# Optimization experiments

Hardware: AMD Instinct MI355X
Metric: run time of the kernel (lower is better)

## Reference

```python
import jax, jax.numpy as jnp
import numpy as np

DK = 64
DROPOUT_P = 0.1


def setup_inputs() -> dict:
    key = jax.random.key(0)
    kq, kk, kv, km = jax.random.split(key, 4)
    B, S, D = 16, 2048, 64
    q = jax.random.normal(kq, (B, S, D), dtype=jnp.float32)
    k = jax.random.normal(kk, (B, S, D), dtype=jnp.float32)
    v = jax.random.normal(kv, (B, S, D), dtype=jnp.float32)
    attn_mask = jax.random.randint(km, (S, S), 0, 2, dtype=jnp.int32)
    return {"q": q, "k": k, "v": v, "attn_mask": attn_mask}


def reference(q, k, v, attn_mask):
    # q = q / sqrt(dk)
    qs = q * (1.0 / np.sqrt(DK)).astype(np.float32)
    # dots: [B, S_q, S_k]
    dots = jnp.einsum("bqd,bkd->bqk", qs, k)
    # mask: 0 -> -inf, 1 -> 0 (additive)
    add_mask = jnp.where(attn_mask == 0, -jnp.inf, 0.0).astype(dots.dtype)
    dots = dots + add_mask  # broadcast [S,S] over batch
    attn = jax.nn.softmax(dots, axis=-1)
    # inverted dropout, train mode, fixed key for determinism
    keep = jax.random.bernoulli(jax.random.key(42), 1.0 - DROPOUT_P, attn.shape)
    attn = jnp.where(keep, attn * (1.0 / (1.0 - DROPOUT_P)), 0.0)
    out = jnp.einsum("bqk,bkd->bqd", attn, v)
    return out
```

## Files before the change

### kernel.cpp

```cpp
#include <hip/hip_runtime.h>

#define BATCH 16
#define SEQ   2048
#define DIM   64
#define TQ    64
#define TK    64
#define NTHREADS 256

typedef short bf16x8 __attribute__((ext_vector_type(8)));
typedef float f32x4 __attribute__((ext_vector_type(4)));

__device__ __forceinline__ int ldsoff(int row) {
  return row * 72 + 16 * (row >> 2);
}
#define LDS_SZ (64 * 72 + 16 * 16)

__device__ __forceinline__ unsigned tf_bits(unsigned f) {
  unsigned x0 = 0u;
  unsigned x1 = f;
  const unsigned ks1 = 42u;
  const unsigned ks2 = 0x1BD11BDAu ^ 42u;
  x1 += ks1;
#define TF_R(r) { x0 += x1; x1 = __builtin_amdgcn_alignbit(x1, x1, 32u - (r)); x1 ^= x0; }
  TF_R(13) TF_R(15) TF_R(26) TF_R(6)
  x0 += ks1; x1 += ks2 + 1u;
  TF_R(17) TF_R(29) TF_R(16) TF_R(24)
  x0 += ks2; x1 += 2u;
  TF_R(13) TF_R(15) TF_R(26) TF_R(6)
  x1 += ks1 + 3u;
  TF_R(17) TF_R(29) TF_R(16) TF_R(24)
  x0 += ks1; x1 += ks2 + 4u;
  TF_R(13) TF_R(15) TF_R(26) TF_R(6)
  x0 += ks2; x1 += 5u;
#undef TF_R
  return x0 ^ x1;
}
#define KEEP_THRESH 0xE6666600u

__device__ __forceinline__ unsigned short to_bf16(float x) {
  return (unsigned short)((__float_as_uint(x) + 0x8000u) >> 16);
}
__device__ __forceinline__ unsigned pack_bf16x2(float lo, float hi) {
  const unsigned l = (__float_as_uint(lo) + 0x8000u) >> 16;
  const unsigned h = (__float_as_uint(hi) + 0x8000u) & 0xFFFF0000u;
  return h | l;
}

__global__ __launch_bounds__(NTHREADS, 2)
void attn_fwd(const float* __restrict__ q, const float* __restrict__ k,
              const float* __restrict__ v, const int* __restrict__ mask,
              float* __restrict__ out) {
  __shared__ unsigned short KS[LDS_SZ];
  __shared__ unsigned short VT[LDS_SZ];
  __shared__ unsigned short PS[LDS_SZ];

  const int t    = threadIdx.x;
  const int w    = t >> 6;
  const int lane = t & 63;
  const int tx   = lane & 15;
  const int quad = lane >> 4;
  const int bb   = blockIdx.x >> 5;
  const int q0   = (blockIdx.x & 31) * TQ;
  const int qw   = q0 + 16 * w;

  const float qscale = 0.125f * 1.44269504088896340736f;

  bf16x8 aq[2];
  {
    const float* qr = q + ((size_t)bb * SEQ + qw + tx) * DIM + quad * 8;
#pragma unroll
    for (int ks = 0; ks < 2; ++ks) {
      const float4 f0 = *(const float4*)(qr + ks * 32);
      const float4 f1 = *(const float4*)(qr + ks * 32 + 4);
      union { unsigned u[4]; bf16x8 v; } a;
      a.u[0] = pack_bf16x2(f0.x * qscale, f0.y * qscale);
      a.u[1] = pack_bf16x2(f0.z * qscale, f0.w * qscale);
      a.u[2] = pack_bf16x2(f1.x * qscale, f1.y * qscale);
      a.u[3] = pack_bf16x2(f1.z * qscale, f1.w * qscale);
      aq[ks] = a.v;
    }
  }

  float mrun[4] = {-3.0e4f, -3.0e4f, -3.0e4f, -3.0e4f};
  float lrun[4] = {0.f, 0.f, 0.f, 0.f};
  f32x4 oacc[4];
#pragma unroll
  for (int nt = 0; nt < 4; ++nt) oacc[nt] = (f32x4){0.f, 0.f, 0.f, 0.f};

  const int srow0 = t >> 4;
  const int sdd   = (t & 15) * 4;
  const float* kb = k + (size_t)bb * SEQ * DIM;
  const float* vb = v + (size_t)bb * SEQ * DIM;

  float4 kreg[4], vreg[4];
#pragma unroll
  for (int p = 0; p < 4; ++p) {
    const int rr = p * 16 + srow0;
    kreg[p] = *(const float4*)(kb + (size_t)rr * DIM + sdd);
    vreg[p] = *(const float4*)(vb + (size_t)rr * DIM + sdd);
  }

  const int* mbase = mask + (size_t)(qw + quad * 4) * SEQ + tx;
  const unsigned fbase0 = (unsigned)(bb * SEQ + qw + quad * 4) * (unsigned)SEQ + (unsigned)tx;

#pragma unroll 1
  for (int kt = 0; kt < SEQ / TK; ++kt) {
    const int k0 = kt * TK;

    __syncthreads();

#pragma unroll
    for (int p = 0; p < 4; ++p) {
      const int rr = p * 16 + srow0;
      ushort4 kk4;
      kk4.x = to_bf16(kreg[p].x); kk4.y = to_bf16(kreg[p].y);
      kk4.z = to_bf16(kreg[p].z); kk4.w = to_bf16(kreg[p].w);
      *(ushort4*)&KS[ldsoff(rr) + sdd] = kk4;
      VT[ldsoff(sdd + 0) + rr] = to_bf16(vreg[p].x);
      VT[ldsoff(sdd + 1) + rr] = to_bf16(vreg[p].y);
      VT[ldsoff(sdd + 2) + rr] = to_bf16(vreg[p].z);
      VT[ldsoff(sdd + 3) + rr] = to_bf16(vreg[p].w);
    }
    __syncthreads();

    if (kt + 1 < SEQ / TK) {
      const size_t off = (size_t)(k0 + TK) * DIM;
#pragma unroll
      for (int p = 0; p < 4; ++p) {
        const int rr = p * 16 + srow0;
        kreg[p] = *(const float4*)(kb + off + (size_t)rr * DIM + sdd);
        vreg[p] = *(const float4*)(vb + off + (size_t)rr * DIM + sdd);
      }
    }

    int mv[4][4];
    const int* mp0 = mbase + k0;
#pragma unroll
    for (int reg = 0; reg < 4; ++reg)
#pragma unroll
      for (int nt = 0; nt < 4; ++nt)
        mv[nt][reg] = mp0[(size_t)reg * SEQ + nt * 16];

    f32x4 qk[4];
#pragma unroll
    for (int nt = 0; nt < 4; ++nt) {
      f32x4 c = (f32x4){0.f, 0.f, 0.f, 0.f};
#pragma unroll
      for (int ks = 0; ks < 2; ++ks) {
        const bf16x8 b = *(const bf16x8*)&KS[ldsoff(nt * 16 + tx) + ks * 32 + quad * 8];
        c = __builtin_amdgcn_mfma_f32_16x16x32_bf16(aq[ks], b, c, 0, 0, 0);
      }
      qk[nt] = c;
    }

    float al[4];
#pragma unroll
    for (int reg = 0; reg < 4; ++reg) {
#pragma unroll
      for (int nt = 0; nt < 4; ++nt)
        qk[nt][reg] = mv[nt][reg] ? qk[nt][reg] : -1e30f;
      float mx = fmaxf(fmaxf(qk[0][reg], qk[1][reg]), fmaxf(qk[2][reg], qk[3][reg]));
      mx = fmaxf(mx, __shfl_xor(mx, 1));
      mx = fmaxf(mx, __shfl_xor(mx, 2));
      mx = fmaxf(mx, __shfl_xor(mx, 4));
      mx = fmaxf(mx, __shfl_xor(mx, 8));
      const float mn = fmaxf(mrun[reg], mx);
      al[reg] = __builtin_amdgcn_exp2f(mrun[reg] - mn);
      mrun[reg] = mn;
    }

    const unsigned fb = fbase0 + (unsigned)k0;
#pragma unroll
    for (int reg = 0; reg < 4; ++reg) {
      const float mn = mrun[reg];
      const int prow = ldsoff(16 * w + quad * 4 + reg);
      float ls = 0.0f;
#pragma unroll
      for (int nt = 0; nt < 4; ++nt) {
        const float e = __builtin_amdgcn_exp2f(qk[nt][reg] - mn);
        ls += e;
        const unsigned bits = tf_bits(fb + (unsigned)(reg * SEQ + nt * 16));
        const float pd = (bits < KEEP_THRESH) ? e : 0.0f;
        PS[prow + nt * 16 + tx] = to_bf16(pd);
      }
      lrun[reg] = lrun[reg] * al[reg] + ls;
    }

#pragma unroll
    for (int nt = 0; nt < 4; ++nt) {
      f32x4 o = oacc[nt];
      o[0] *= al[0]; o[1] *= al[1]; o[2] *= al[2]; o[3] *= al[3];
      oacc[nt] = o;
    }
#pragma unroll
    for (int ks = 0; ks < 2; ++ks) {
      const bf16x8 ap = *(const bf16x8*)&PS[ldsoff(16 * w + tx) + ks * 32 + quad * 8];
#pragma unroll
      for (int nt = 0; nt < 4; ++nt) {
        const bf16x8 bv = *(const bf16x8*)&VT[ldsoff(nt * 16 + tx) + ks * 32 + quad * 8];
        oacc[nt] = __builtin_amdgcn_mfma_f32_16x16x32_bf16(ap, bv, oacc[nt], 0, 0, 0);
      }
    }
  }

  float linv[4];
#pragma unroll
  for (int reg = 0; reg < 4; ++reg) {
    float ls = lrun[reg];
    ls += __shfl_xor(ls, 1);
    ls += __shfl_xor(ls, 2);
    ls += __shfl_xor(ls, 4);
    ls += __shfl_xor(ls, 8);
    linv[reg] = (1.0f / 0.9f) / ls;
  }
  float* ob = out + ((size_t)bb * SEQ + qw) * DIM;
#pragma unroll
  for (int nt = 0; nt < 4; ++nt)
#pragma unroll
    for (int reg = 0; reg < 4; ++reg)
      ob[(size_t)(quad * 4 + reg) * DIM + nt * 16 + tx] = oacc[nt][reg] * linv[reg];
}

extern "C" void kernel_launch(void* const* d_in, const int* in_sizes, int n_in,
                              void* d_out, int out_size, void* d_ws, size_t ws_size,
                              hipStream_t stream) {
  const float* q = (const float*)d_in[0];
  const float* k = (const float*)d_in[1];
  const float* v = (const float*)d_in[2];
  const int* mask = (const int*)d_in[3];
  float* out = (float*)d_out;
  dim3 grid(BATCH * (SEQ / TQ));
  dim3 block(NTHREADS);
  hipLaunchKernelGGL(attn_fwd, grid, block, 0, stream, q, k, v, mask, out);
}
```

Measured before the change: 260.8 us.

## Split KV range across two blocks per query tile and add combine kernel

Splits the key sequence into two halves handled by separate blocks, doubling the grid from 512 to 1024 blocks, and writes partial outputs plus the row max and sum to workspace. A second kernel merges the two partials with log-sum-exp rescaling. It also changes the V loading so each thread writes the transposed V tile with vector LDS stores instead of scalar ones. The aim is to fill more CUs on the device, at the cost of an extra launch and extra global traffic for the partials. The split path runs only when the workspace is large enough, otherwise the original single-pass kernel runs.

```diff
diff --git a/kernel.cpp b/kernel.cpp
--- a/kernel.cpp
+++ b/kernel.cpp
@@ -6,6 +6,8 @@
 #define TQ    64
 #define TK    64
 #define NTHREADS 256
+#define NROWS    (BATCH * SEQ)
+#define OUTELEMS (NROWS * DIM)
 
 typedef short bf16x8 __attribute__((ext_vector_type(8)));
 typedef float f32x4 __attribute__((ext_vector_type(4)));
@@ -46,10 +48,18 @@
   return h | l;
 }
 
+#define WS_M0 0
+#define WS_L0 32768
+#define WS_M1 65536
+#define WS_L1 98304
+#define WS_O1 131072
+#define WS_NEED ((size_t)(WS_O1 + OUTELEMS) * 4)
+
+template <int SPLIT>
 __global__ __launch_bounds__(NTHREADS, 2)
 void attn_fwd(const float* __restrict__ q, const float* __restrict__ k,
               const float* __restrict__ v, const int* __restrict__ mask,
-              float* __restrict__ out) {
+              float* __restrict__ out, float* __restrict__ ws) {
   __shared__ unsigned short KS[LDS_SZ];
   __shared__ unsigned short VT[LDS_SZ];
   __shared__ unsigned short PS[LDS_SZ];
@@ -59,9 +69,24 @@
   const int lane = t & 63;
   const int tx   = lane & 15;
   const int quad = lane >> 4;
-  const int bb   = blockIdx.x >> 5;
-  const int q0   = (blockIdx.x & 31) * TQ;
-  const int qw   = q0 + 16 * w;
+
+  int bid = blockIdx.x;
+  const int half = SPLIT ? (bid >> 9) : 0;
+  bid &= 511;
+  const int bb = bid >> 5;
+  const int q0 = (bid & 31) * TQ;
+  const int qw = q0 + 16 * w;
+  const int kt0 = SPLIT ? half * (SEQ / TK / 2) : 0;
+  const int ktN = SPLIT ? (SEQ / TK / 2) : (SEQ / TK);
+
+  float* optr; float* mptr; float* lptr;
+  if (SPLIT) {
+    optr = half ? (ws + WS_O1) : out;
+    mptr = ws + (half ? WS_M1 : WS_M0);
+    lptr = ws + (half ? WS_L1 : WS_L0);
+  } else {
+    optr = out; mptr = nullptr; lptr = nullptr;
+  }
 
   const float qscale = 0.125f * 1.44269504088896340736f;
 
@@ -89,22 +114,29 @@
 
   const int srow0 = t >> 4;
   const int sdd   = (t & 15) * 4;
+  const int s4    = srow0 * 4;
   const float* kb = k + (size_t)bb * SEQ * DIM;
   const float* vb = v + (size_t)bb * SEQ * DIM;
 
-  float4 kreg[4], vreg[4];
-#pragma unroll
-  for (int p = 0; p < 4; ++p) {
-    const int rr = p * 16 + srow0;
-    kreg[p] = *(const float4*)(kb + (size_t)rr * DIM + sdd);
-    vreg[p] = *(const float4*)(vb + (size_t)rr * DIM + sdd);
+  float4 kreg[4];
+  float  vr[4][4];
+  {
+    const size_t off0 = (size_t)kt0 * TK * DIM;
+#pragma unroll
+    for (int p = 0; p < 4; ++p)
+      kreg[p] = *(const float4*)(kb + off0 + (size_t)(p * 16 + srow0) * DIM + sdd);
+#pragma unroll
+    for (int i = 0; i < 4; ++i) {
+      const float4 t4 = *(const float4*)(vb + off0 + (size_t)(s4 + i) * DIM + sdd);
+      vr[i][0] = t4.x; vr[i][1] = t4.y; vr[i][2] = t4.z; vr[i][3] = t4.w;
+    }
   }
 
   const int* mbase = mask + (size_t)(qw + quad * 4) * SEQ + tx;
   const unsigned fbase0 = (unsigned)(bb * SEQ + qw + quad * 4) * (unsigned)SEQ + (unsigned)tx;
 
 #pragma unroll 1
-  for (int kt = 0; kt < SEQ / TK; ++kt) {
+  for (int kt = kt0; kt < kt0 + ktN; ++kt) {
     const int k0 = kt * TK;
 
     __syncthreads();
@@ -116,20 +148,25 @@
       kk4.x = to_bf16(kreg[p].x); kk4.y = to_bf16(kreg[p].y);
       kk4.z = to_bf16(kreg[p].z); kk4.w = to_bf16(kreg[p].w);
       *(ushort4*)&KS[ldsoff(rr) + sdd] = kk4;
-      VT[ldsoff(sdd + 0) + rr] = to_bf16(vreg[p].x);
-      VT[ldsoff(sdd + 1) + rr] = to_bf16(vreg[p].y);
-      VT[ldsoff(sdd + 2) + rr] = to_bf16(vreg[p].z);
-      VT[ldsoff(sdd + 3) + rr] = to_bf16(vreg[p].w);
+    }
+#pragma unroll
+    for (int c = 0; c < 4; ++c) {
+      ushort4 tv;
+      tv.x = to_bf16(vr[0][c]); tv.y = to_bf16(vr[1][c]);
+      tv.z = to_bf16(vr[2][c]); tv.w = to_bf16(vr[3][c]);
+      *(ushort4*)&VT[ldsoff(sdd + c) + s4] = tv;
     }
     __syncthreads();
 
-    if (kt + 1 < SEQ / TK) {
+    if (kt + 1 < kt0 + ktN) {
       const size_t off = (size_t)(k0 + TK) * DIM;
 #pragma unroll
-      for (int p = 0; p < 4; ++p) {
-        const int rr = p * 16 + srow0;
-        kreg[p] = *(const float4*)(kb + off + (size_t)rr * DIM + sdd);
-        vreg[p] = *(const float4*)(vb + off + (size_t)rr * DIM + sdd);
+      for (int p = 0; p < 4; ++p)
+        kreg[p] = *(const float4*)(kb + off + (size_t)(p * 16 + srow0) * DIM + sdd);
+#pragma unroll
+      for (int i = 0; i < 4; ++i) {
+        const float4 t4 = *(const float4*)(vb + off + (size_t)(s4 + i) * DIM + sdd);
+        vr[i][0] = t4.x; vr[i][1] = t4.y; vr[i][2] = t4.z; vr[i][3] = t4.w;
       }
     }
 
@@ -203,7 +240,7 @@
     }
   }
 
-  float linv[4];
+  float lred[4];
 #pragma unroll
   for (int reg = 0; reg < 4; ++reg) {
     float ls = lrun[reg];
@@ -211,14 +248,45 @@
     ls += __shfl_xor(ls, 2);
     ls += __shfl_xor(ls, 4);
     ls += __shfl_xor(ls, 8);
-    linv[reg] = (1.0f / 0.9f) / ls;
-  }
-  float* ob = out + ((size_t)bb * SEQ + qw) * DIM;
-#pragma unroll
-  for (int nt = 0; nt < 4; ++nt)
-#pragma unroll
-    for (int reg = 0; reg < 4; ++reg)
-      ob[(size_t)(quad * 4 + reg) * DIM + nt * 16 + tx] = oacc[nt][reg] * linv[reg];
+    lred[reg] = ls;
+  }
+  float* ob = optr + ((size_t)bb * SEQ + qw) * DIM;
+  if (SPLIT) {
+    if (tx == 0) {
+#pragma unroll
+      for (int reg = 0; reg < 4; ++reg) {
+        const int grow = bb * SEQ + qw + quad * 4 + reg;
+        mptr[grow] = mrun[reg];
+        lptr[grow] = lred[reg];
+      }
+    }
+#pragma unroll
+    for (int nt = 0; nt < 4; ++nt)
+#pragma unroll
+      for (int reg = 0; reg < 4; ++reg)
+        ob[(size_t)(quad * 4 + reg) * DIM + nt * 16 + tx] = oacc[nt][reg];
+  } else {
+#pragma unroll
+    for (int nt = 0; nt < 4; ++nt)
+#pragma unroll
+      for (int reg = 0; reg < 4; ++reg)
+        ob[(size_t)(quad * 4 + reg) * DIM + nt * 16 + tx] =
+            oacc[nt][reg] * ((1.0f / 0.9f) / lred[reg]);
+  }
+}
+
+__global__ __launch_bounds__(NTHREADS)
+void combine(float* __restrict__ out, const float* __restrict__ ws) {
+  const int gid = blockIdx.x * NTHREADS + threadIdx.x;
+  const int row = gid >> 6;
+  const float m0 = ws[WS_M0 + row], l0 = ws[WS_L0 + row];
+  const float m1 = ws[WS_M1 + row], l1 = ws[WS_L1 + row];
+  const float M  = fmaxf(m0, m1);
+  const float w0 = __builtin_amdgcn_exp2f(m0 - M);
+  const float w1 = __builtin_amdgcn_exp2f(m1 - M);
+  const float num = out[gid] * w0 + ws[WS_O1 + gid] * w1;
+  const float den = 0.9f * (l0 * w0 + l1 * w1);
+  out[gid] = num / den;
 }
 
 extern "C" void kernel_launch(void* const* d_in, const int* in_sizes, int n_in,
@@ -229,7 +297,14 @@
   const float* v = (const float*)d_in[2];
   const int* mask = (const int*)d_in[3];
   float* out = (float*)d_out;
-  dim3 grid(BATCH * (SEQ / TQ));
-  dim3 block(NTHREADS);
-  hipLaunchKernelGGL(attn_fwd, grid, block, 0, stream, q, k, v, mask, out);
-}
+  float* ws = (float*)d_ws;
+  if (ws_size >= WS_NEED) {
+    hipLaunchKernelGGL(attn_fwd<1>, dim3(1024), dim3(NTHREADS), 0, stream,
+                       q, k, v, mask, out, ws);
+    hipLaunchKernelGGL(combine, dim3(OUTELEMS / NTHREADS), dim3(NTHREADS), 0, stream,
+                       out, ws);
+  } else {
+    hipLaunchKernelGGL(attn_fwd<0>, dim3(512), dim3(NTHREADS), 0, stream,
+                       q, k, v, mask, out, ws);
+  }
+}
```

Result: faster. 251.3 us (-3.6%).
